# Performance work log

Hardware: AMD Instinct MI355X
Metric: run time of the kernel (lower is better)

## Reference

```python
import jax, jax.numpy as jnp
import numpy as np

N_NODES = 50000
N_EDGES = 800000
N_GRAPHS = 64
IN_CH = 128
GLOBAL_DIM = 256
HIDDEN = 64
HEADS = 4
N_CLASSES = 10


def setup_inputs() -> dict:
    key = jax.random.key(0)
    ks = jax.random.split(key, 32)
    lin = lambda k, fi, fo: jax.random.normal(k, (fi, fo), jnp.float32) * 0.02
    inp = {}
    inp["x"] = jax.random.normal(ks[0], (N_NODES, IN_CH), jnp.float32)
    inp["edge_index"] = jax.random.randint(ks[1], (2, N_EDGES), 0, N_NODES)
    inp["batch"] = jnp.sort(jax.random.randint(ks[2], (N_NODES,), 0, N_GRAPHS))
    inp["global_feats"] = jax.random.normal(ks[3], (N_GRAPHS, GLOBAL_DIM), jnp.float32)
    # conv1 (in=IN_CH)
    inp["c1_Wq"] = lin(ks[4], IN_CH, HEADS * HIDDEN); inp["c1_bq"] = jnp.zeros((HEADS * HIDDEN,), jnp.float32)
    inp["c1_Wk"] = lin(ks[5], IN_CH, HEADS * HIDDEN); inp["c1_bk"] = jnp.zeros((HEADS * HIDDEN,), jnp.float32)
    inp["c1_Wv"] = lin(ks[6], IN_CH, HEADS * HIDDEN); inp["c1_bv"] = jnp.zeros((HEADS * HIDDEN,), jnp.float32)
    inp["c1_Ws"] = lin(ks[7], IN_CH, HIDDEN);         inp["c1_bs"] = jnp.zeros((HIDDEN,), jnp.float32)
    # conv2 (in=HIDDEN)
    inp["c2_Wq"] = lin(ks[8], HIDDEN, HEADS * HIDDEN); inp["c2_bq"] = jnp.zeros((HEADS * HIDDEN,), jnp.float32)
    inp["c2_Wk"] = lin(ks[9], HIDDEN, HEADS * HIDDEN); inp["c2_bk"] = jnp.zeros((HEADS * HIDDEN,), jnp.float32)
    inp["c2_Wv"] = lin(ks[10], HIDDEN, HEADS * HIDDEN); inp["c2_bv"] = jnp.zeros((HEADS * HIDDEN,), jnp.float32)
    inp["c2_Ws"] = lin(ks[11], HIDDEN, HIDDEN);         inp["c2_bs"] = jnp.zeros((HIDDEN,), jnp.float32)
    # global MLP
    inp["g_W1"] = lin(ks[12], GLOBAL_DIM, HIDDEN); inp["g_b1"] = jnp.zeros((HIDDEN,), jnp.float32)
    inp["g_W2"] = lin(ks[13], HIDDEN, HIDDEN);     inp["g_b2"] = jnp.zeros((HIDDEN,), jnp.float32)
    # head
    inp["h_W1"] = lin(ks[14], 2 * HIDDEN, HIDDEN); inp["h_b1"] = jnp.zeros((HIDDEN,), jnp.float32)
    inp["h_W2"] = lin(ks[15], HIDDEN, N_CLASSES); inp["h_b2"] = jnp.zeros((N_CLASSES,), jnp.float32)
    return inp


def _tconv(x, src, dst, Wq, bq, Wk, bk, Wv, bv, Ws, bs):
    """PyG TransformerConv, heads=HEADS, concat=False (head-mean), root skip, eval-mode (no dropout)."""
    N = x.shape[0]
    q = (x @ Wq + bq).reshape(N, HEADS, HIDDEN)
    k = (x @ Wk + bk).reshape(N, HEADS, HIDDEN)
    v = (x @ Wv + bv).reshape(N, HEADS, HIDDEN)
    # per-edge attention logits  [E, H]
    s = jnp.einsum('ehd,ehd->eh', q[dst], k[src]) / jnp.sqrt(jnp.float32(HIDDEN))
    # segment softmax over incoming edges of each dst node
    m = jax.ops.segment_max(s, dst, num_segments=N)           # [N, H]
    e = jnp.exp(s - m[dst])                                    # [E, H]
    z = jax.ops.segment_sum(e, dst, num_segments=N)           # [N, H]
    alpha = e / z[dst]                                         # [E, H] (dst always has >=1 edge here)
    agg = jax.ops.segment_sum(alpha[:, :, None] * v[src], dst, num_segments=N)  # [N, H, D]
    return agg.mean(axis=1) + x @ Ws + bs


def reference(x, edge_index, batch, global_feats,
              c1_Wq, c1_bq, c1_Wk, c1_bk, c1_Wv, c1_bv, c1_Ws, c1_bs,
              c2_Wq, c2_bq, c2_Wk, c2_bk, c2_Wv, c2_bv, c2_Ws, c2_bs,
              g_W1, g_b1, g_W2, g_b2, h_W1, h_b1, h_W2, h_b2):
    src, dst = edge_index[0], edge_index[1]
    h = jax.nn.relu(_tconv(x, src, dst, c1_Wq, c1_bq, c1_Wk, c1_bk, c1_Wv, c1_bv, c1_Ws, c1_bs))
    h = jax.nn.relu(_tconv(h, src, dst, c2_Wq, c2_bq, c2_Wk, c2_bk, c2_Wv, c2_bv, c2_Ws, c2_bs))
    # global mean pool per graph
    ssum = jax.ops.segment_sum(h, batch, num_segments=N_GRAPHS)                # [G, HIDDEN]
    cnt = jax.ops.segment_sum(jnp.ones((h.shape[0],), h.dtype), batch, num_segments=N_GRAPHS)
    patch_emb = ssum / jnp.maximum(cnt, 1.0)[:, None]
    g = jax.nn.relu(global_feats @ g_W1 + g_b1)
    g = jax.nn.relu(g @ g_W2 + g_b2)
    fused = jnp.concatenate([patch_emb, g], axis=-1)
    return jax.nn.relu(fused @ h_W1 + h_b1) @ h_W2 + h_b2
```

## Files before the change

kernel.cpp:

```cpp
#include <hip/hip_runtime.h>
#include <hip/hip_bf16.h>
#include <math.h>

#define N_NODES   50000
#define N_EDGES   800000
#define N_GRAPHS  64
#define IN_CH     128
#define GLOBAL_DIM 256
#define HIDDEN    64
#define HEADS     4
#define N_CLASSES 10
#define QKV_COLS  832
#define MAXDEG    64

#define P1B    128
#define EPB    6250
#define NBUCK  196
#define SLABP  80

typedef unsigned short ushort_t;
typedef unsigned int uint_t;
typedef unsigned char uchar_t;
typedef __attribute__((ext_vector_type(8))) short short8;
typedef __attribute__((ext_vector_type(4))) float floatx4;
typedef __attribute__((ext_vector_type(2))) float floatx2;

__device__ __forceinline__ ushort_t bf16rne(float f) {
    uint_t b = __float_as_uint(f);
    b += 0x7fffu + ((b >> 16) & 1u);
    return (ushort_t)(b >> 16);
}
__device__ __forceinline__ float4 bf4_unpack(uint_t lo, uint_t hi) {
    float4 f;
    f.x = __uint_as_float(lo << 16);
    f.y = __uint_as_float(lo & 0xffff0000u);
    f.z = __uint_as_float(hi << 16);
    f.w = __uint_as_float(hi & 0xffff0000u);
    return f;
}
__device__ __forceinline__ uchar_t fp8e4m3(float f) {
    int v = __builtin_amdgcn_cvt_pk_fp8_f32(f, 0.f, 0, false);
    return (uchar_t)(v & 0xff);
}
__device__ __forceinline__ short8 pack_bf8(float4 a, float4 b) {
    union { short8 s; ushort_t u[8]; } r;
    r.u[0] = bf16rne(a.x); r.u[1] = bf16rne(a.y);
    r.u[2] = bf16rne(a.z); r.u[3] = bf16rne(a.w);
    r.u[4] = bf16rne(b.x); r.u[5] = bf16rne(b.y);
    r.u[6] = bf16rne(b.z); r.u[7] = bf16rne(b.w);
    return r.s;
}
__device__ __forceinline__ void graph_range(const int* __restrict__ batch, int g,
                                            int& start, int& end) {
    int lo = 0, hi = N_NODES;
    while (lo < hi) { int mid = (lo + hi) >> 1; if (batch[mid] < g) lo = mid + 1; else hi = mid; }
    start = lo;
    hi = N_NODES;
    while (lo < hi) { int mid = (lo + hi) >> 1; if (batch[mid] < g + 1) lo = mid + 1; else hi = mid; }
    end = lo;
}

#define PREP_CONC_B  624

__global__ __launch_bounds__(256) void prep_p1(
        const float* __restrict__ W1q, const float* __restrict__ W1k,
        const float* __restrict__ W1v, const float* __restrict__ W1s,
        const float* __restrict__ b1q, const float* __restrict__ b1k,
        const float* __restrict__ b1v, const float* __restrict__ b1s,
        const float* __restrict__ W2q, const float* __restrict__ W2k,
        const float* __restrict__ W2v, const float* __restrict__ W2s,
        const float* __restrict__ b2q, const float* __restrict__ b2k,
        const float* __restrict__ b2v, const float* __restrict__ b2s,
        ushort_t* __restrict__ Wt1, ushort_t* __restrict__ Wt2,
        float* __restrict__ bcat1, float* __restrict__ bcat2,
        const int* __restrict__ src, const int* __restrict__ dst,
        uint_t* __restrict__ slab, int* __restrict__ cntm) {
    int b = blockIdx.x, t = threadIdx.x;
    if (b >= PREP_CONC_B) {
        int blk = b - PREP_CONC_B;
        __shared__ int hist[NBUCK];
        for (int i = t; i < NBUCK; i += 256) hist[i] = 0;
        __syncthreads();
        int e0 = blk * EPB;
        int e1 = e0 + EPB;
        for (int e = e0 + t; e < e1; e += 256) {
            int s = src[e], d = dst[e];
            int bu = d >> 8;
            int off = atomicAdd(&hist[bu], 1);
            if (off < SLABP)
                slab[((size_t)bu * P1B + blk) * SLABP + off] =
                    ((uint_t)d << 16) | (uint_t)s;
        }
        __syncthreads();
        for (int i = t; i < NBUCK; i += 256)
            cntm[i * P1B + blk] = hist[i] < SLABP ? hist[i] : SLABP;
        return;
    }
    int idx = b * 256 + t;
    const int T1 = IN_CH * QKV_COLS;
    const int T2 = HIDDEN * QKV_COLS;
    if (idx < T1) {
        int c = idx / IN_CH, k = idx % IN_CH;
        float v;
        if (c < 256)      v = W1q[k * 256 + c];
        else if (c < 512) v = W1k[k * 256 + (c - 256)];
        else if (c < 768) v = W1v[k * 256 + (c - 512)];
        else              v = W1s[k * 64  + (c - 768)];
        Wt1[idx] = bf16rne(v);
    } else if (idx < T1 + T2) {
        int i2 = idx - T1;
        int c = i2 / HIDDEN, k = i2 % HIDDEN;
        float v;
        if (c < 256)      v = W2q[k * 256 + c];
        else if (c < 512) v = W2k[k * 256 + (c - 256)];
        else if (c < 768) v = W2v[k * 256 + (c - 512)];
        else              v = W2s[k * 64  + (c - 768)];
        Wt2[i2] = bf16rne(v);
    }
    if (idx < QKV_COLS) {
        float bb, b2;
        if (idx < 256)      { bb = b1q[idx];       b2 = b2q[idx]; }
        else if (idx < 512) { bb = b1k[idx - 256]; b2 = b2k[idx - 256]; }
        else if (idx < 768) { bb = b1v[idx - 512]; b2 = b2v[idx - 512]; }
        else                { bb = b1s[idx - 768]; b2 = b2s[idx - 768]; }
        bcat1[idx] = bb;
        bcat2[idx] = b2;
    }
}

template <int K, bool A_FP32>
__device__ __forceinline__ void gemm_body9(int idx0, int t,
                                           const void* __restrict__ Av,
                                           const ushort_t* __restrict__ Wt,
                                           const float* __restrict__ bias,
                                           uchar_t* __restrict__ qb8,
                                           uchar_t* __restrict__ kvb,
                                           ushort_t* __restrict__ skipb,
                                           int N, int RB, uchar_t* smem) {
    constexpr int KP = K + 8;
    constexpr int C8 = K / 8;
    ushort_t* Bs = (ushort_t*)smem;

    const int xcd = idx0 & 7;
    const int j = idx0 >> 3;
    const int ct = j % 13;
    const int strip = (j / 13) * 8 + xcd;
    if (strip >= RB) return;
    const int base_r = strip * 128;
    const int base_c = ct * 64;

#pragma unroll
    for (int i = 0; i < (64 * C8) / 256; ++i) {
        int ii = t + i * 256;
        int n = ii / C8, c = ii % C8;
        *(uint4*)(Bs + n * KP + c * 8) =
            *(const uint4*)(Wt + (size_t)(base_c + n) * K + c * 8);
    }

    const int wave = t >> 6, lane = t & 63;
    const int quad = lane >> 4, m16 = lane & 15;

    int arow0 = base_r + wave * 32 + m16;
    int arow1 = arow0 + 16;
    int cr0 = arow0 < N ? arow0 : N - 1;
    int cr1 = arow1 < N ? arow1 : N - 1;
    short8 a0[K / 32], a1[K / 32];
    if (A_FP32) {
        const float* A = (const float*)Av;
        const float* Ar0 = A + (size_t)cr0 * K + quad * 8;
        const float* Ar1 = A + (size_t)cr1 * K + quad * 8;
#pragma unroll
        for (int kc = 0; kc < K / 32; ++kc) {
            float4 f0 = *(const float4*)(Ar0 + kc * 32);
            float4 f1 = *(const float4*)(Ar0 + kc * 32 + 4);
            a0[kc] = pack_bf8(f0, f1);
            float4 g0 = *(const float4*)(Ar1 + kc * 32);
            float4 g1 = *(const float4*)(Ar1 + kc * 32 + 4);
            a1[kc] = pack_bf8(g0, g1);
        }
    } else {
        const ushort_t* A = (const ushort_t*)Av;
        const ushort_t* Ar0 = A + (size_t)cr0 * K + quad * 8;
        const ushort_t* Ar1 = A + (size_t)cr1 * K + quad * 8;
#pragma unroll
        for (int kc = 0; kc < K / 32; ++kc) {
            a0[kc] = *(const short8*)(Ar0 + kc * 32);
            a1[kc] = *(const short8*)(Ar1 + kc * 32);
        }
    }
    __syncthreads();

    floatx4 acc[2][4];
#pragma unroll
    for (int rt = 0; rt < 2; ++rt)
#pragma unroll
        for (int c2 = 0; c2 < 4; ++c2) acc[rt][c2] = (floatx4){0.f, 0.f, 0.f, 0.f};
#pragma unroll
    for (int kc = 0; kc < K / 32; ++kc) {
        int ko = kc * 32 + quad * 8;
#pragma unroll
        for (int c2 = 0; c2 < 4; ++c2) {
            short8 b = *(const short8*)(Bs + (c2 * 16 + m16) * KP + ko);
            acc[0][c2] = __builtin_amdgcn_mfma_f32_16x16x32_bf16(a0[kc], b, acc[0][c2], 0, 0, 0);
            acc[1][c2] = __builtin_amdgcn_mfma_f32_16x16x32_bf16(a1[kc], b, acc[1][c2], 0, 0, 0);
        }
    }

    float bb[4];
#pragma unroll
    for (int c2 = 0; c2 < 4; ++c2) bb[c2] = bias[base_c + c2 * 16 + m16];
#pragma unroll
    for (int rt = 0; rt < 2; ++rt)
#pragma unroll
        for (int c2 = 0; c2 < 4; ++c2)
#pragma unroll
            for (int r = 0; r < 4; ++r) acc[rt][c2][r] += bb[c2];

    __syncthreads();

    if (ct < 12) {
        uchar_t* ep = smem;
#pragma unroll
        for (int c2 = 0; c2 < 4; ++c2) {
            int col_l = c2 * 16 + m16;
#pragma unroll
            for (int rt = 0; rt < 2; ++rt)
#pragma unroll
                for (int r = 0; r < 4; ++r)
                    ep[(wave * 32 + rt * 16 + quad * 4 + r) * 80 + col_l] =
                        fp8e4m3(acc[rt][c2][r]);
        }
        __syncthreads();
        if (ct < 4) {
#pragma unroll
            for (int i = 0; i < 2; ++i) {
                int ii = t + i * 256;
                int row = ii >> 2, ch = ii & 3;
                int gr = base_r + row;
                if (gr < N)
                    *(uint4*)(qb8 + (size_t)gr * 256 + base_c + ch * 16) =
                        *(const uint4*)(ep + row * 80 + ch * 16);
            }
        } else {
            const bool isv = (ct >= 8);
            const int dim0base = isv ? (base_c - 512) : (base_c - 256);
            const int vo = isv ? 8 : 0;
#pragma unroll
            for (int i = 0; i < 2; ++i) {
                int ii = t + i * 256;
                int row = ii >> 2, ch = ii & 3;
                int gr = base_r + row;
                int cb = ((dim0base + ch * 16) << 1) + vo;
                if (gr < N) {
                    *(uint2*)(kvb + (size_t)gr * 512 + cb) =
                        *(const uint2*)(ep + row * 80 + ch * 16);
                    *(uint2*)(kvb + (size_t)gr * 512 + cb + 16) =
                        *(const uint2*)(ep + row * 80 + ch * 16 + 8);
                }
            }
        }
    } else {
        ushort_t* ep = (ushort_t*)smem;
#pragma unroll
        for (int c2 = 0; c2 < 4; ++c2) {
            int col_l = c2 * 16 + m16;
#pragma unroll
            for (int rt = 0; rt < 2; ++rt)
#pragma unroll
                for (int r = 0; r < 4; ++r)
                    ep[(wave * 32 + rt * 16 + quad * 4 + r) * 68 + col_l] =
                        bf16rne(acc[rt][c2][r]);
        }
        __syncthreads();
#pragma unroll
        for (int i = 0; i < 4; ++i) {
            int ii = t + i * 256;
            int row = ii >> 3, ch = ii & 7;
            int gr = base_r + row;
            if (gr < N)
                *(uint4*)(skipb + (size_t)gr * 64 + ch * 8) =
                    *(const uint4*)(ep + row * 68 + ch * 8);
        }
    }
}

template <int K, bool A_FP32>
__global__ __launch_bounds__(256) void gemm_fill9(const void* __restrict__ Av,
                                                  const ushort_t* __restrict__ Wt,
                                                  const float* __restrict__ bias,
                                                  uchar_t* __restrict__ qb8,
                                                  uchar_t* __restrict__ kvb,
                                                  ushort_t* __restrict__ skipb,
                                                  int N, int RB,
                                                  const int* __restrict__ cntm,
                                                  const uint_t* __restrict__ slab,
                                                  int* __restrict__ deg,
                                                  ushort_t* __restrict__ col) {
    __shared__ uchar_t smem[17408] __attribute__((aligned(16)));
    int t = threadIdx.x;
    int idx = (int)blockIdx.x;
    if (idx < NBUCK) {
        __shared__ int cnt2[256];
        __shared__ int cs[P1B];
        if (t < P1B) cs[t] = cntm[idx * P1B + t];
        cnt2[t] = 0;
        __syncthreads();
        const uint_t* myslab = slab + (size_t)idx * P1B * SLABP;
        for (int i = t; i < P1B * SLABP; i += 256) {
            int blkq = i / SLABP;
            int off = i - blkq * SLABP;
            if (off < cs[blkq]) {
                uint_t rec = myslab[i];
                int d = rec >> 16;
                int pos = atomicAdd(&cnt2[d & 255], 1);
                col[((size_t)d << 6) + pos] = (ushort_t)(rec & 0xffffu);
            }
        }
        __syncthreads();
        int gn = (idx << 8) + t;
        if (gn < N_NODES) deg[gn] = cnt2[t];
        return;
    }
    gemm_body9<K, A_FP32>(idx - NBUCK, t, Av, Wt, bias, qb8, kvb, skipb, N, RB, smem);
}

template <int K, bool A_FP32>
__global__ __launch_bounds__(256) void gemm_v9(const void* __restrict__ Av,
                                               const ushort_t* __restrict__ Wt,
                                               const float* __restrict__ bias,
                                               uchar_t* __restrict__ qb8,
                                               uchar_t* __restrict__ kvb,
                                               ushort_t* __restrict__ skipb,
                                               int N, int RB) {
    __shared__ uchar_t smem[17408] __attribute__((aligned(16)));
    gemm_body9<K, A_FP32>((int)blockIdx.x, threadIdx.x, Av, Wt, bias,
                          qb8, kvb, skipb, N, RB, smem);
}

__device__ __forceinline__ void edge_step3(uint2 k8, uint2 v8, const floatx2* qp,
                                           float& z, floatx2* acp) {
    floatx2 dp = qp[0] * __builtin_amdgcn_cvt_pk_f32_fp8(k8.x, false);
    dp += qp[1] * __builtin_amdgcn_cvt_pk_f32_fp8(k8.x, true);
    dp += qp[2] * __builtin_amdgcn_cvt_pk_f32_fp8(k8.y, false);
    dp += qp[3] * __builtin_amdgcn_cvt_pk_f32_fp8(k8.y, true);
    float d = dp[0] + dp[1];
    d += __shfl_xor(d, 1);
    d += __shfl_xor(d, 2);
    d += __shfl_xor(d, 4);
    float p = __expf(d);
    z += p;
    floatx2 pp = {p, p};
    acp[0] += pp * __builtin_amdgcn_cvt_pk_f32_fp8(v8.x, false);
    acp[1] += pp * __builtin_amdgcn_cvt_pk_f32_fp8(v8.x, true);
    acp[2] += pp * __builtin_amdgcn_cvt_pk_f32_fp8(v8.y, false);
    acp[3] += pp * __builtin_amdgcn_cvt_pk_f32_fp8(v8.y, true);
}

template <bool OUT_BF16>
__global__ __launch_bounds__(256) void attn_agg7(const uchar_t* __restrict__ qb8,
                                                 const uchar_t* __restrict__ kvb,
                                                 const ushort_t* __restrict__ skipb,
                                                 const int* __restrict__ deg,
                                                 const ushort_t* __restrict__ col,
                                                 void* __restrict__ hout) {
    int node = blockIdx.x * 4 + threadIdx.y;
    if (node >= N_NODES) return;
    int lane = threadIdx.x;
    int half = lane >> 5, sl = lane & 31;
    uint2 qd = *(const uint2*)(qb8 + (size_t)node * 256 + sl * 8);
    const floatx2 s8 = {0.125f, 0.125f};
    floatx2 qp[4];
    qp[0] = s8 * __builtin_amdgcn_cvt_pk_f32_fp8(qd.x, false);
    qp[1] = s8 * __builtin_amdgcn_cvt_pk_f32_fp8(qd.x, true);
    qp[2] = s8 * __builtin_amdgcn_cvt_pk_f32_fp8(qd.y, false);
    qp[3] = s8 * __builtin_amdgcn_cvt_pk_f32_fp8(qd.y, true);
    floatx2 acp[4];
    acp[0] = (floatx2){0.f, 0.f}; acp[1] = (floatx2){0.f, 0.f};
    acp[2] = (floatx2){0.f, 0.f}; acp[3] = (floatx2){0.f, 0.f};
    float z = 0.f;
    int dv = deg[node];
    int creg = (int)col[(node << 6) | lane];
    int e = half;
    const uchar_t* kb = kvb + (size_t)sl * 16;
    for (; e + 6 < dv; e += 8) {
        int c0 = __shfl(creg, e);
        int c1 = __shfl(creg, e + 2);
        int c2 = __shfl(creg, e + 4);
        int c3 = __shfl(creg, e + 6);
        uint4 x0 = *(const uint4*)(kb + (size_t)c0 * 512);
        uint4 x1 = *(const uint4*)(kb + (size_t)c1 * 512);
        uint4 x2 = *(const uint4*)(kb + (size_t)c2 * 512);
        uint4 x3 = *(const uint4*)(kb + (size_t)c3 * 512);
        edge_step3(make_uint2(x0.x, x0.y), make_uint2(x0.z, x0.w), qp, z, acp);
        edge_step3(make_uint2(x1.x, x1.y), make_uint2(x1.z, x1.w), qp, z, acp);
        edge_step3(make_uint2(x2.x, x2.y), make_uint2(x2.z, x2.w), qp, z, acp);
        edge_step3(make_uint2(x3.x, x3.y), make_uint2(x3.z, x3.w), qp, z, acp);
    }
    for (; e < dv; e += 2) {
        int c0 = __shfl(creg, e);
        uint4 x0 = *(const uint4*)(kb + (size_t)c0 * 512);
        edge_step3(make_uint2(x0.x, x0.y), make_uint2(x0.z, x0.w), qp, z, acp);
    }
    z += __shfl_xor(z, 32);
    float ac[8] = {acp[0][0], acp[0][1], acp[1][0], acp[1][1],
                   acp[2][0], acp[2][1], acp[3][0], acp[3][1]};
#pragma unroll
    for (int i = 0; i < 8; ++i) ac[i] += __shfl_xor(ac[i], 32);
    float inv = (z > 0.f) ? (0.25f / z) : 0.f;
#pragma unroll
    for (int i = 0; i < 8; ++i) ac[i] *= inv;
#pragma unroll
    for (int i = 0; i < 8; ++i) {
        ac[i] += __shfl_xor(ac[i], 8);
        ac[i] += __shfl_xor(ac[i], 16);
    }
    if (lane < 8) {
        uint4 su = *(const uint4*)(skipb + (size_t)node * 64 + lane * 8);
        float4 s0 = bf4_unpack(su.x, su.y);
        float4 s1 = bf4_unpack(su.z, su.w);
        float o0 = fmaxf(ac[0] + s0.x, 0.f);
        float o1 = fmaxf(ac[1] + s0.y, 0.f);
        float o2 = fmaxf(ac[2] + s0.z, 0.f);
        float o3 = fmaxf(ac[3] + s0.w, 0.f);
        float o4 = fmaxf(ac[4] + s1.x, 0.f);
        float o5 = fmaxf(ac[5] + s1.y, 0.f);
        float o6 = fmaxf(ac[6] + s1.z, 0.f);
        float o7 = fmaxf(ac[7] + s1.w, 0.f);
        if (OUT_BF16) {
            uint4 u;
            u.x = (uint_t)bf16rne(o0) | ((uint_t)bf16rne(o1) << 16);
            u.y = (uint_t)bf16rne(o2) | ((uint_t)bf16rne(o3) << 16);
            u.z = (uint_t)bf16rne(o4) | ((uint_t)bf16rne(o5) << 16);
            u.w = (uint_t)bf16rne(o6) | ((uint_t)bf16rne(o7) << 16);
            *(uint4*)((ushort_t*)hout + (size_t)node * HIDDEN + lane * 8) = u;
        } else {
            float* op = (float*)hout + (size_t)node * HIDDEN + lane * 8;
            *(float4*)(op)     = make_float4(o0, o1, o2, o3);
            *(float4*)(op + 4) = make_float4(o4, o5, o6, o7);
        }
    }
}

__global__ __launch_bounds__(256) void pool_partial(const float* __restrict__ h,
                                                    const int* __restrict__ batch,
                                                    float* __restrict__ part) {
    int g = blockIdx.x >> 3;
    int s = blockIdx.x & 7;
    int start, end;
    graph_range(batch, g, start, end);
    int len = end - start;
    int s0 = start + (len * s) / 8;
    int s1 = start + (len * (s + 1)) / 8;
    int t = threadIdx.x;
    int d = t & 63, chunk = t >> 6;
    float acc = 0.f;
    for (int n = s0 + chunk; n < s1; n += 4) acc += h[(size_t)n * HIDDEN + d];
    __shared__ float sh[256];
    sh[t] = acc;
    __syncthreads();
    if (t < 64)
        part[(size_t)blockIdx.x * 64 + t] = sh[t] + sh[64 + t] + sh[128 + t] + sh[192 + t];
}

__global__ __launch_bounds__(256) void head_mlp(const float* __restrict__ part,
                                                const int* __restrict__ batch,
                                                const float* __restrict__ gf,
                                                const float* __restrict__ gW1, const float* __restrict__ gb1,
                                                const float* __restrict__ gW2, const float* __restrict__ gb2,
                                                const float* __restrict__ hW1, const float* __restrict__ hb1,
                                                const float* __restrict__ hW2, const float* __restrict__ hb2,
                                                float* __restrict__ out) {
    int g = blockIdx.x;
    int t = threadIdx.x;
    int d = t & 63, kk = t >> 6;
    int start, end;
    graph_range(batch, g, start, end);
    float cnt = fmaxf((float)(end - start), 1.0f);
    __shared__ float gfs[GLOBAL_DIM];
    __shared__ float fused[2 * HIDDEN];
    __shared__ float g1[HIDDEN];
    __shared__ float h1s[HIDDEN];
    __shared__ float red[256];
    gfs[t] = gf[(size_t)g * GLOBAL_DIM + t];
    if (t < 64) {
        float s = 0.f;
#pragma unroll
        for (int i = 0; i < 8; ++i) s += part[((size_t)g * 8 + i) * 64 + t];
        fused[t] = s / cnt;
    }
    __syncthreads();
    {
        float a = 0.f;
        int k0 = kk * 64;
#pragma unroll 4
        for (int k = k0; k < k0 + 64; ++k) a = fmaf(gfs[k], gW1[k * HIDDEN + d], a);
        red[t] = a;
        __syncthreads();
        if (t < 64) g1[t] = fmaxf(red[t] + red[64 + t] + red[128 + t] + red[192 + t] + gb1[t], 0.f);
        __syncthreads();
    }
    {
        float a = 0.f;
        int k0 = kk * 16;
#pragma unroll 4
        for (int k = k0; k < k0 + 16; ++k) a = fmaf(g1[k], gW2[k * HIDDEN + d], a);
        red[t] = a;
        __syncthreads();
        if (t < 64) fused[HIDDEN + t] =
            fmaxf(red[t] + red[64 + t] + red[128 + t] + red[192 + t] + gb2[t], 0.f);
        __syncthreads();
    }
    {
        float a = 0.f;
        int k0 = kk * 32;
#pragma unroll 4
        for (int k = k0; k < k0 + 32; ++k) a = fmaf(fused[k], hW1[k * HIDDEN + d], a);
        red[t] = a;
        __syncthreads();
        if (t < 64) h1s[t] = fmaxf(red[t] + red[64 + t] + red[128 + t] + red[192 + t] + hb1[t], 0.f);
        __syncthreads();
    }
    if (t < N_CLASSES) {
        float o = hb2[t];
#pragma unroll 4
        for (int k = 0; k < HIDDEN; ++k) o = fmaf(h1s[k], hW2[k * N_CLASSES + t], o);
        out[(size_t)g * N_CLASSES + t] = o;
    }
}

extern "C" void kernel_launch(void* const* d_in, const int* in_sizes, int n_in,
                              void* d_out, int out_size, void* d_ws, size_t ws_size,
                              hipStream_t stream) {
    const float* x        = (const float*)d_in[0];
    const int*   eidx     = (const int*)d_in[1];
    const int*   batch    = (const int*)d_in[2];
    const float* gfeats   = (const float*)d_in[3];
    const float* c1_Wq = (const float*)d_in[4];  const float* c1_bq = (const float*)d_in[5];
    const float* c1_Wk = (const float*)d_in[6];  const float* c1_bk = (const float*)d_in[7];
    const float* c1_Wv = (const float*)d_in[8];  const float* c1_bv = (const float*)d_in[9];
    const float* c1_Ws = (const float*)d_in[10]; const float* c1_bs = (const float*)d_in[11];
    const float* c2_Wq = (const float*)d_in[12]; const float* c2_bq = (const float*)d_in[13];
    const float* c2_Wk = (const float*)d_in[14]; const float* c2_bk = (const float*)d_in[15];
    const float* c2_Wv = (const float*)d_in[16]; const float* c2_bv = (const float*)d_in[17];
    const float* c2_Ws = (const float*)d_in[18]; const float* c2_bs = (const float*)d_in[19];
    const float* g_W1 = (const float*)d_in[20]; const float* g_b1 = (const float*)d_in[21];
    const float* g_W2 = (const float*)d_in[22]; const float* g_b2 = (const float*)d_in[23];
    const float* h_W1 = (const float*)d_in[24]; const float* h_b1 = (const float*)d_in[25];
    const float* h_W2 = (const float*)d_in[26]; const float* h_b2 = (const float*)d_in[27];
    float* out = (float*)d_out;

    const int* srcp = eidx;
    const int* dstp = eidx + N_EDGES;

    char* base = (char*)d_ws;
    uchar_t*  kvb  = (uchar_t*)base;  base += (size_t)N_NODES * 512;
    uchar_t*  qb8  = (uchar_t*)base;  base += (size_t)N_NODES * 256;
    ushort_t* skipb = (ushort_t*)base; base += (size_t)N_NODES * HIDDEN * 2;
    ushort_t* h1b  = (ushort_t*)base; base += (size_t)N_NODES * HIDDEN * 2;
    float*    h2   = (float*)base;    base += (size_t)N_NODES * HIDDEN * 4;
    ushort_t* Wt1  = (ushort_t*)base; base += (size_t)IN_CH * QKV_COLS * 2;
    ushort_t* Wt2  = (ushort_t*)base; base += (size_t)HIDDEN * QKV_COLS * 2;
    float*    bcat1 = (float*)base;   base += QKV_COLS * 4;
    float*    bcat2 = (float*)base;   base += QKV_COLS * 4;
    float*    part = (float*)base;    base += (size_t)N_GRAPHS * 8 * 64 * 4;
    int*      deg  = (int*)base;      base += (size_t)N_NODES * 4;
    ushort_t* colb = (ushort_t*)base; base += ((size_t)N_NODES * MAXDEG + 64) * 2;

    uint_t* slab = (uint_t*)h2;
    int*    cntm = (int*)((char*)h2 + (size_t)NBUCK * P1B * SLABP * 4);

    const int RB = (N_NODES + 127) / 128;
    const int GG = 8 * 13 * ((RB + 7) / 8);
    dim3 attn_block(64, 4);
    int attn_grid = (N_NODES + 3) / 4;

    prep_p1<<<PREP_CONC_B + P1B, 256, 0, stream>>>(
        c1_Wq, c1_Wk, c1_Wv, c1_Ws, c1_bq, c1_bk, c1_bv, c1_bs,
        c2_Wq, c2_Wk, c2_Wv, c2_Ws, c2_bq, c2_bk, c2_bv, c2_bs,
        Wt1, Wt2, bcat1, bcat2, srcp, dstp, slab, cntm);

    gemm_fill9<IN_CH, true><<<NBUCK + GG, 256, 0, stream>>>(
        x, Wt1, bcat1, qb8, kvb, skipb, N_NODES, RB, cntm, slab, deg, colb);
    attn_agg7<true><<<attn_grid, attn_block, 0, stream>>>(qb8, kvb, skipb, deg, colb, h1b);

    gemm_v9<HIDDEN, false><<<GG, 256, 0, stream>>>(h1b, Wt2, bcat2, qb8, kvb, skipb, N_NODES, RB);
    attn_agg7<false><<<attn_grid, attn_block, 0, stream>>>(qb8, kvb, skipb, deg, colb, h2);

    pool_partial<<<N_GRAPHS * 8, 256, 0, stream>>>(h2, batch, part);
    head_mlp<<<N_GRAPHS, 256, 0, stream>>>(part, batch, gfeats,
                                           g_W1, g_b1, g_W2, g_b2,
                                           h_W1, h_b1, h_W2, h_b2, out);
}
```

Baseline: 353.2 us.

## Widen QKV GEMM column tiles to 128 and rebalance edge bucketing blocks

The fused QKV/skip GEMM now uses 128-column tiles (7 column groups instead of 13 per row strip), so each block reuses its loaded A rows across twice as many output columns. This cuts redundant A-row reads and block count. In exchange it needs more LDS and accumulator registers, which may lower occupancy. Separately, the edge bucketing phase uses twice as many blocks with half the edges each and a smaller per-bucket slab.

New measurement: 343.2 us. 1.03x faster.

```diff
diff --git a/kernel.cpp b/kernel.cpp
--- a/kernel.cpp
+++ b/kernel.cpp
@@ -13,10 +13,10 @@
 #define QKV_COLS  832
 #define MAXDEG    64
 
-#define P1B    128
-#define EPB    6250
+#define P1B    256
+#define EPB    3125
 #define NBUCK  196
-#define SLABP  80
+#define SLABP  48
 
 typedef unsigned short ushort_t;
 typedef unsigned int uint_t;
@@ -129,32 +129,34 @@
 }
 
 template <int K, bool A_FP32>
-__device__ __forceinline__ void gemm_body9(int idx0, int t,
-                                           const void* __restrict__ Av,
-                                           const ushort_t* __restrict__ Wt,
-                                           const float* __restrict__ bias,
-                                           uchar_t* __restrict__ qb8,
-                                           uchar_t* __restrict__ kvb,
-                                           ushort_t* __restrict__ skipb,
-                                           int N, int RB, uchar_t* smem) {
+__device__ __forceinline__ void gemm_body11(int idx0, int t,
+                                            const void* __restrict__ Av,
+                                            const ushort_t* __restrict__ Wt,
+                                            const float* __restrict__ bias,
+                                            uchar_t* __restrict__ qb8,
+                                            uchar_t* __restrict__ kvb,
+                                            ushort_t* __restrict__ skipb,
+                                            int N, int RB, uchar_t* smem) {
     constexpr int KP = K + 8;
     constexpr int C8 = K / 8;
     ushort_t* Bs = (ushort_t*)smem;
 
     const int xcd = idx0 & 7;
     const int j = idx0 >> 3;
-    const int ct = j % 13;
-    const int strip = (j / 13) * 8 + xcd;
+    const int g = j % 7;
+    const int strip = (j / 7) * 8 + xcd;
     if (strip >= RB) return;
     const int base_r = strip * 128;
-    const int base_c = ct * 64;
-
-#pragma unroll
-    for (int i = 0; i < (64 * C8) / 256; ++i) {
+    const int NC = (g < 6) ? 128 : 64;
+    const int base_c = (g < 6) ? g * 128 : 768;
+
+#pragma unroll
+    for (int i = 0; i < (128 * C8) / 256; ++i) {
         int ii = t + i * 256;
         int n = ii / C8, c = ii % C8;
-        *(uint4*)(Bs + n * KP + c * 8) =
-            *(const uint4*)(Wt + (size_t)(base_c + n) * K + c * 8);
+        if (n < NC)
+            *(uint4*)(Bs + n * KP + c * 8) =
+                *(const uint4*)(Wt + (size_t)(base_c + n) * K + c * 8);
     }
 
     const int wave = t >> 6, lane = t & 63;
@@ -190,76 +192,97 @@
     }
     __syncthreads();
 
-    floatx4 acc[2][4];
-#pragma unroll
-    for (int rt = 0; rt < 2; ++rt)
-#pragma unroll
-        for (int c2 = 0; c2 < 4; ++c2) acc[rt][c2] = (floatx4){0.f, 0.f, 0.f, 0.f};
-#pragma unroll
-    for (int kc = 0; kc < K / 32; ++kc) {
-        int ko = kc * 32 + quad * 8;
-#pragma unroll
-        for (int c2 = 0; c2 < 4; ++c2) {
-            short8 b = *(const short8*)(Bs + (c2 * 16 + m16) * KP + ko);
-            acc[0][c2] = __builtin_amdgcn_mfma_f32_16x16x32_bf16(a0[kc], b, acc[0][c2], 0, 0, 0);
-            acc[1][c2] = __builtin_amdgcn_mfma_f32_16x16x32_bf16(a1[kc], b, acc[1][c2], 0, 0, 0);
-        }
-    }
-
-    float bb[4];
-#pragma unroll
-    for (int c2 = 0; c2 < 4; ++c2) bb[c2] = bias[base_c + c2 * 16 + m16];
-#pragma unroll
-    for (int rt = 0; rt < 2; ++rt)
-#pragma unroll
-        for (int c2 = 0; c2 < 4; ++c2)
-#pragma unroll
-            for (int r = 0; r < 4; ++r) acc[rt][c2][r] += bb[c2];
-
-    __syncthreads();
-
-    if (ct < 12) {
+    if (g < 6) {
+        floatx4 acc[2][8];
+#pragma unroll
+        for (int rt = 0; rt < 2; ++rt)
+#pragma unroll
+            for (int c2 = 0; c2 < 8; ++c2) acc[rt][c2] = (floatx4){0.f, 0.f, 0.f, 0.f};
+#pragma unroll
+        for (int kc = 0; kc < K / 32; ++kc) {
+            int ko = kc * 32 + quad * 8;
+#pragma unroll
+            for (int c2 = 0; c2 < 8; ++c2) {
+                short8 b = *(const short8*)(Bs + (c2 * 16 + m16) * KP + ko);
+                acc[0][c2] = __builtin_amdgcn_mfma_f32_16x16x32_bf16(a0[kc], b, acc[0][c2], 0, 0, 0);
+                acc[1][c2] = __builtin_amdgcn_mfma_f32_16x16x32_bf16(a1[kc], b, acc[1][c2], 0, 0, 0);
+            }
+        }
+        float bb[8];
+#pragma unroll
+        for (int c2 = 0; c2 < 8; ++c2) bb[c2] = bias[base_c + c2 * 16 + m16];
+#pragma unroll
+        for (int rt = 0; rt < 2; ++rt)
+#pragma unroll
+            for (int c2 = 0; c2 < 8; ++c2)
+#pragma unroll
+                for (int r = 0; r < 4; ++r) acc[rt][c2][r] += bb[c2];
+
+        __syncthreads();
+
         uchar_t* ep = smem;
 #pragma unroll
-        for (int c2 = 0; c2 < 4; ++c2) {
+        for (int c2 = 0; c2 < 8; ++c2) {
             int col_l = c2 * 16 + m16;
 #pragma unroll
             for (int rt = 0; rt < 2; ++rt)
 #pragma unroll
                 for (int r = 0; r < 4; ++r)
-                    ep[(wave * 32 + rt * 16 + quad * 4 + r) * 80 + col_l] =
+                    ep[(wave * 32 + rt * 16 + quad * 4 + r) * 144 + col_l] =
                         fp8e4m3(acc[rt][c2][r]);
         }
         __syncthreads();
-        if (ct < 4) {
-#pragma unroll
-            for (int i = 0; i < 2; ++i) {
+        if (g < 2) {
+#pragma unroll
+            for (int i = 0; i < 4; ++i) {
                 int ii = t + i * 256;
-                int row = ii >> 2, ch = ii & 3;
+                int row = ii >> 3, ch = ii & 7;
                 int gr = base_r + row;
                 if (gr < N)
-                    *(uint4*)(qb8 + (size_t)gr * 256 + base_c + ch * 16) =
-                        *(const uint4*)(ep + row * 80 + ch * 16);
+                    *(uint4*)(qb8 + (size_t)gr * 256 + g * 128 + ch * 16) =
+                        *(const uint4*)(ep + row * 144 + ch * 16);
             }
         } else {
-            const bool isv = (ct >= 8);
-            const int dim0base = isv ? (base_c - 512) : (base_c - 256);
-            const int vo = isv ? 8 : 0;
-#pragma unroll
-            for (int i = 0; i < 2; ++i) {
+            const int half = (g & 1);
+            const int vo = (g >= 4) ? 8 : 0;
+#pragma unroll
+            for (int i = 0; i < 8; ++i) {
                 int ii = t + i * 256;
-                int row = ii >> 2, ch = ii & 3;
+                int row = ii >> 4, ch = ii & 15;
                 int gr = base_r + row;
-                int cb = ((dim0base + ch * 16) << 1) + vo;
-                if (gr < N) {
-                    *(uint2*)(kvb + (size_t)gr * 512 + cb) =
-                        *(const uint2*)(ep + row * 80 + ch * 16);
-                    *(uint2*)(kvb + (size_t)gr * 512 + cb + 16) =
-                        *(const uint2*)(ep + row * 80 + ch * 16 + 8);
-                }
+                if (gr < N)
+                    *(uint2*)(kvb + (size_t)gr * 512 + half * 256 + ch * 16 + vo) =
+                        *(const uint2*)(ep + row * 144 + ch * 8);
             }
         }
     } else {
+        floatx4 acc[2][4];
+#pragma unroll
+        for (int rt = 0; rt < 2; ++rt)
+#pragma unroll
+            for (int c2 = 0; c2 < 4; ++c2) acc[rt][c2] = (floatx4){0.f, 0.f, 0.f, 0.f};
+#pragma unroll
+        for (int kc = 0; kc < K / 32; ++kc) {
+            int ko = kc * 32 + quad * 8;
+#pragma unroll
+            for (int c2 = 0; c2 < 4; ++c2) {
+                short8 b = *(const short8*)(Bs + (c2 * 16 + m16) * KP + ko);
+                acc[0][c2] = __builtin_amdgcn_mfma_f32_16x16x32_bf16(a0[kc], b, acc[0][c2], 0, 0, 0);
+                acc[1][c2] = __builtin_amdgcn_mfma_f32_16x16x32_bf16(a1[kc], b, acc[1][c2], 0, 0, 0);
+            }
+        }
+        float bb[4];
+#pragma unroll
+        for (int c2 = 0; c2 < 4; ++c2) bb[c2] = bias[768 + c2 * 16 + m16];
+#pragma unroll
+        for (int rt = 0; rt < 2; ++rt)
+#pragma unroll
+            for (int c2 = 0; c2 < 4; ++c2)
+#pragma unroll
+                for (int r = 0; r < 4; ++r) acc[rt][c2][r] += bb[c2];
+
+        __syncthreads();
+
         ushort_t* ep = (ushort_t*)smem;
 #pragma unroll
         for (int c2 = 0; c2 < 4; ++c2) {
@@ -296,7 +319,7 @@
                                                   const uint_t* __restrict__ slab,
                                                   int* __restrict__ deg,
                                                   ushort_t* __restrict__ col) {
-    __shared__ uchar_t smem[17408] __attribute__((aligned(16)));
+    __shared__ uchar_t smem[(K == 128) ? 34816 : 18432] __attribute__((aligned(16)));
     int t = threadIdx.x;
     int idx = (int)blockIdx.x;
     if (idx < NBUCK) {
@@ -321,7 +344,7 @@
         if (gn < N_NODES) deg[gn] = cnt2[t];
         return;
     }
-    gemm_body9<K, A_FP32>(idx - NBUCK, t, Av, Wt, bias, qb8, kvb, skipb, N, RB, smem);
+    gemm_body11<K, A_FP32>(idx - NBUCK, t, Av, Wt, bias, qb8, kvb, skipb, N, RB, smem);
 }
 
 template <int K, bool A_FP32>
@@ -332,9 +355,9 @@
                                                uchar_t* __restrict__ kvb,
                                                ushort_t* __restrict__ skipb,
                                                int N, int RB) {
-    __shared__ uchar_t smem[17408] __attribute__((aligned(16)));
-    gemm_body9<K, A_FP32>((int)blockIdx.x, threadIdx.x, Av, Wt, bias,
-                          qb8, kvb, skipb, N, RB, smem);
+    __shared__ uchar_t smem[(K == 128) ? 34816 : 18432] __attribute__((aligned(16)));
+    gemm_body11<K, A_FP32>((int)blockIdx.x, threadIdx.x, Av, Wt, bias,
+                           qb8, kvb, skipb, N, RB, smem);
 }
 
 __device__ __forceinline__ void edge_step3(uint2 k8, uint2 v8, const floatx2* qp,
@@ -570,7 +593,7 @@
     int*    cntm = (int*)((char*)h2 + (size_t)NBUCK * P1B * SLABP * 4);
 
     const int RB = (N_NODES + 127) / 128;
-    const int GG = 8 * 13 * ((RB + 7) / 8);
+    const int GG = 8 * 7 * ((RB + 7) / 8);
     dim3 attn_block(64, 4);
     int attn_grid = (N_NODES + 3) / 4;
 
```
